# Kernel optimization log

Hardware: AMD Instinct MI355X
Metric: run time of the kernel (lower is better)

## Reference

```python
import jax, jax.numpy as jnp
import numpy as np

N = 50000      # nodes (particles)
E = 1600000    # edges
G = 2000       # graphs (jets)
NEG_SLOPE = 0.2

def setup_inputs() -> dict:
    key = jax.random.key(0)
    ks = jax.random.split(key, 18)
    p = lambda k, s: (jax.random.normal(k, s, jnp.float32) * 0.1)
    return {
        'x': jax.random.normal(ks[0], (N, 3), jnp.float32),
        'edge_index': jax.random.randint(ks[1], (2, E), 0, N, dtype=jnp.int64),
        'batch': jnp.sort(jax.random.randint(ks[2], (N,), 0, G, dtype=jnp.int64)),
        'W1': p(ks[3], (3, 128)),  'a1s': p(ks[4], (4, 32)),  'a1d': p(ks[5], (4, 32)),  'b1': p(ks[6], (128,)),
        'W2': p(ks[7], (128, 128)),'a2s': p(ks[8], (4, 32)),  'a2d': p(ks[9], (4, 32)),  'b2': p(ks[10], (128,)),
        'W3': p(ks[11], (128, 32)),'a3s': p(ks[12], (1, 32)), 'a3d': p(ks[13], (1, 32)), 'b3': p(ks[14], (32,)),
        'Wh': p(ks[15], (32, 2)),  'bh': p(ks[16], (2,)),
    }

def gat_conv(x, src, dst, W, a_src, a_dst, b, concat):
    """PyG GATConv (eval mode): gather-score-softmax-scatter over edges (src->dst)."""
    n = x.shape[0]
    H, C = a_src.shape
    h = (x @ W).reshape(n, H, C)                         # [N,H,C]
    es = jnp.sum(h * a_src, axis=-1)                     # [N,H] source scores
    ed = jnp.sum(h * a_dst, axis=-1)                     # [N,H] dest scores
    e = jax.nn.leaky_relu(es[src] + ed[dst], NEG_SLOPE)  # [E,H]
    # neighbor-wise (per destination node) stable softmax
    m = jax.ops.segment_max(e, dst, num_segments=n)      # [N,H]
    m = jax.lax.stop_gradient(jnp.where(jnp.isfinite(m), m, 0.0))
    w = jnp.exp(e - m[dst])
    z = jax.ops.segment_sum(w, dst, num_segments=n)      # [N,H]
    alpha = w / (z[dst] + 1e-16)                         # [E,H]
    out = jax.ops.segment_sum(h[src] * alpha[:, :, None], dst, num_segments=n)  # [N,H,C]
    out = out.reshape(n, H * C) if concat else out.mean(axis=1)
    return out + b

def reference(x, edge_index, batch, W1, a1s, a1d, b1, W2, a2s, a2d, b2,
              W3, a3s, a3d, b3, Wh, bh):
    n = x.shape[0]
    loops = jnp.arange(n, dtype=edge_index.dtype)        # add_self_loops=True
    src = jnp.concatenate([edge_index[0], loops])
    dst = jnp.concatenate([edge_index[1], loops])
    h = jax.nn.elu(gat_conv(x, src, dst, W1, a1s, a1d, b1, True))
    h = jax.nn.elu(gat_conv(h, src, dst, W2, a2s, a2d, b2, True))
    h = jax.nn.elu(gat_conv(h, src, dst, W3, a3s, a3d, b3, False))
    cnt = jax.ops.segment_sum(jnp.ones((n,), h.dtype), batch, num_segments=G)
    pooled = jax.ops.segment_sum(h, batch, num_segments=G) / jnp.maximum(cnt, 1.0)[:, None]
    return pooled @ Wh + bh                              # [G, n_classes]
```

## Files before the change

kernel.cpp:

```cpp
#include <hip/hip_runtime.h>

#define CAP 80
#define NXCD 8
#define SUBW 128
#define NSUBR 49
#define SQC 96
#define QCAPB 512
#define CHUNK 2048

typedef int vint4 __attribute__((ext_vector_type(4)));
__device__ __forceinline__ vint4 ntload_i4(const int* p){ return __builtin_nontemporal_load((const vint4*)p); }

__device__ __forceinline__ float lrelu02(float x){ return x > 0.f ? x : 0.2f*x; }
__device__ __forceinline__ float eluf(float x){ return x > 0.f ? x : (__expf(x)-1.f); }
__device__ __forceinline__ unsigned short f2bf(float x){
  unsigned u = __float_as_uint(x);
  u += 0x7fffu + ((u >> 16) & 1u);
  return (unsigned short)(u >> 16);
}
__device__ __forceinline__ float bf2f(unsigned short b){
  return __uint_as_float(((unsigned)b) << 16);
}

__global__ void radix_proj1_kernel(const int* __restrict__ src, const int* __restrict__ dst,
                                   int E, int n, int nrb, int RW, int qcap,
                                   int* __restrict__ gcur, int2* __restrict__ qbuf,
                                   const float* __restrict__ x, const float* __restrict__ W,
                                   const float* __restrict__ as_, const float* __restrict__ ad_,
                                   unsigned short* __restrict__ hout, float* __restrict__ es,
                                   float* __restrict__ ed){
  if ((int)blockIdx.x < nrb){
    __shared__ int2 q[NXCD][QCAPB];
    __shared__ int qc[NXCD];
    __shared__ int qbase[NXCD];
    int t = threadIdx.x;
    if (t < NXCD) qc[t] = 0;
    __syncthreads();
    int e0 = blockIdx.x*CHUNK + t*8;
    if (e0 + 8 <= E){
      vint4 d40 = ntload_i4(dst + e0), d41 = ntload_i4(dst + e0 + 4);
      vint4 s40 = ntload_i4(src + e0), s41 = ntload_i4(src + e0 + 4);
      int dd[8] = {d40[0],d40[1],d40[2],d40[3],d41[0],d41[1],d41[2],d41[3]};
      int ss[8] = {s40[0],s40[1],s40[2],s40[3],s41[0],s41[1],s41[2],s41[3]};
      #pragma unroll
      for (int k = 0; k < 8; ++k){
        int qi = min(dd[k] / RW, NXCD-1);
        int pos = atomicAdd(&qc[qi], 1);
        if (pos < QCAPB) q[qi][pos] = make_int2(ss[k], dd[k]);
      }
    } else {
      for (int e = e0; e < E; ++e){
        int d = dst[e];
        int qi = min(d / RW, NXCD-1);
        int pos = atomicAdd(&qc[qi], 1);
        if (pos < QCAPB) q[qi][pos] = make_int2(src[e], d);
      }
    }
    __syncthreads();
    if (t < NXCD) qbase[t] = atomicAdd(&gcur[t], min(qc[t], QCAPB));
    __syncthreads();
    #pragma unroll
    for (int qi = 0; qi < NXCD; ++qi){
      int cq = min(qc[qi], QCAPB);
      int2* gq = qbuf + (size_t)qi*qcap;
      int b0 = qbase[qi];
      for (int i = t; i < cq; i += 256)
        if (b0 + i < qcap) gq[b0 + i] = q[qi][i];
    }
  } else {
    __shared__ float xs[2][3];
    int node0 = ((int)blockIdx.x - nrb) * 2;
    int t = threadIdx.x;
    if (t < 6){
      int nn = node0 + t/3;
      xs[t/3][t%3] = (nn < n) ? x[(size_t)nn*3 + t%3] : 0.f;
    }
    __syncthreads();
    int node = node0 + t / 128;
    int o = t % 128;
    if (node >= n) return;
    const float* xr = xs[t / 128];
    float acc = 0.f;
    #pragma unroll
    for (int k = 0; k < 3; ++k) acc = fmaf(xr[k], W[k*128 + o], acc);
    hout[(size_t)node*128 + o] = f2bf(acc);
    float ts = acc * as_[o];
    float td = acc * ad_[o];
    #pragma unroll
    for (int m = 16; m >= 1; m >>= 1){
      ts += __shfl_xor(ts, m);
      td += __shfl_xor(td, m);
    }
    if ((o & 31) == 0){
      es[node*4 + (o>>5)] = ts;
      ed[node*4 + (o>>5)] = td;
    }
  }
}

__global__ void radix_sub_kernel(const int2* __restrict__ qbuf, const int* __restrict__ gcur,
                                 int qcap, int bpr, int scap,
                                 int* __restrict__ scnt, int2* __restrict__ sbuf){
  __shared__ int2 q[NSUBR][SQC];
  __shared__ int qc[NSUBR];
  __shared__ int qb[NSUBR];
  int r  = blockIdx.x / bpr;
  int bi = blockIdx.x % bpr;
  int t = threadIdx.x;
  if (t < NSUBR) qc[t] = 0;
  __syncthreads();
  int len = min(gcur[r], qcap);
  int i0 = bi*CHUNK + t*8;
  const int2* qg = qbuf + (size_t)r*qcap;
  #pragma unroll
  for (int k = 0; k < 8; ++k){
    int i = i0 + k;
    if (i < len){
      int2 e = qg[i];
      int qi = (e.y >> 7) - r*NSUBR;
      int pos = atomicAdd(&qc[qi], 1);
      if (pos < SQC) q[qi][pos] = e;
    }
  }
  __syncthreads();
  if (t < NSUBR){
    int c = min(qc[t], SQC);
    qb[t] = c ? atomicAdd(&scnt[r*NSUBR + t], c) : 0;
  }
  __syncthreads();
  for (int qi = 0; qi < NSUBR; ++qi){
    int cq = min(qc[qi], SQC);
    if (!cq) continue;
    int2* gq = sbuf + (size_t)(r*NSUBR + qi)*scap;
    int b0 = qb[qi];
    for (int i = t; i < cq; i += 256)
      if (b0 + i < scap) gq[b0 + i] = q[qi][i];
  }
}

__global__ void bucket_csr_kernel(const int2* __restrict__ sbuf, const int* __restrict__ scnt,
                                  int scap, unsigned short* __restrict__ col,
                                  int* __restrict__ deg, int n){
  __shared__ unsigned short colS[SUBW*CAP];
  __shared__ int cur[SUBW];
  int sb = blockIdx.x;
  int t = threadIdx.x;
  if (t < SUBW) cur[t] = 0;
  __syncthreads();
  int len = min(scnt[sb], scap);
  const int2* sq = sbuf + (size_t)sb*scap;
  for (int i = t; i < len; i += 256){
    int2 e = sq[i];
    int r = e.y & (SUBW-1);
    int slot = atomicAdd(&cur[r], 1);
    if (slot < CAP) colS[r*CAP + slot] = (unsigned short)e.x;
  }
  __syncthreads();
  int base = sb*SUBW;
  int nb = min(SUBW, n - base);
  const uint4* srcp = (const uint4*)colS;
  uint4* dstp = (uint4*)(col + (size_t)base*CAP);
  for (int i = t; i < nb*10; i += 256) dstp[i] = srcp[i];
  if (t < nb) deg[base + t] = min(cur[t], CAP);
}

template<int OUT, int NPT, int H>
__global__ void proj_tiled_kernel(const float* __restrict__ x, const float* __restrict__ W,
                                  const float* __restrict__ as_, const float* __restrict__ ad_,
                                  unsigned short* __restrict__ hout, float* __restrict__ es,
                                  float* __restrict__ ed, int n){
  constexpr int OG = OUT / 4;
  constexpr int NG = 256 / OG;
  constexpr int NODES = NG * NPT;
  __shared__ float xs[128][NODES + 1];
  int node0 = blockIdx.x * NODES;
  int t = threadIdx.x;
  for (int i = t; i < NODES*32; i += 256){
    int nl = i >> 5, kc = i & 31;
    int nn = node0 + nl;
    float4 v = make_float4(0.f,0.f,0.f,0.f);
    if (nn < n) v = *(const float4*)(x + (size_t)nn*128 + kc*4);
    xs[kc*4+0][nl] = v.x;
    xs[kc*4+1][nl] = v.y;
    xs[kc*4+2][nl] = v.z;
    xs[kc*4+3][nl] = v.w;
  }
  __syncthreads();
  int og = t % OG;
  int ng = t / OG;
  float acc[NPT][4];
  #pragma unroll
  for (int p = 0; p < NPT; ++p){ acc[p][0]=0.f; acc[p][1]=0.f; acc[p][2]=0.f; acc[p][3]=0.f; }
  const float* wp = W + og*4;
  #pragma unroll 4
  for (int k = 0; k < 128; ++k){
    float4 w = *(const float4*)(wp + (size_t)k*OUT);
    #pragma unroll
    for (int p = 0; p < NPT; ++p){
      float xv = xs[k][ng*NPT + p];
      acc[p][0] = fmaf(xv, w.x, acc[p][0]);
      acc[p][1] = fmaf(xv, w.y, acc[p][1]);
      acc[p][2] = fmaf(xv, w.z, acc[p][2]);
      acc[p][3] = fmaf(xv, w.w, acc[p][3]);
    }
  }
  int o = og*4;
  float as0 = as_[o], as1 = as_[o+1], as2 = as_[o+2], as3 = as_[o+3];
  float ad0 = ad_[o], ad1 = ad_[o+1], ad2 = ad_[o+2], ad3 = ad_[o+3];
  #pragma unroll
  for (int p = 0; p < NPT; ++p){
    int node = node0 + ng*NPT + p;
    float ts = acc[p][0]*as0 + acc[p][1]*as1 + acc[p][2]*as2 + acc[p][3]*as3;
    float td = acc[p][0]*ad0 + acc[p][1]*ad1 + acc[p][2]*ad2 + acc[p][3]*ad3;
    #pragma unroll
    for (int m = 4; m >= 1; m >>= 1){
      ts += __shfl_xor(ts, m);
      td += __shfl_xor(td, m);
    }
    if (node < n){
      ushort4 hb;
      hb.x = f2bf(acc[p][0]); hb.y = f2bf(acc[p][1]);
      hb.z = f2bf(acc[p][2]); hb.w = f2bf(acc[p][3]);
      *(ushort4*)(hout + (size_t)node*OUT + o) = hb;
      if ((og & 7) == 0){
        int head = og >> 3;
        es[node*H + head] = ts;
        ed[node*H + head] = td;
      }
    }
  }
}

__global__ void agg128_kernel(const unsigned short* __restrict__ h, const float* __restrict__ es,
                              const float* __restrict__ ed, const int* __restrict__ deg,
                              const unsigned short* __restrict__ col, const float* __restrict__ bias,
                              float* __restrict__ out, int n){
  int node = blockIdx.x*4 + (threadIdx.x >> 6);
  int lane = threadIdx.x & 63;
  if (node >= n) return;
  int beg = node*CAP;
  int end = beg + min(deg[node], CAP);
  int head = lane >> 4;
  float ed_h = ed[node*4 + head];
  float a0 = 0.f, a1 = 0.f, z = 0.f;
  int e = beg;
  for (; e + 16 <= end; e += 16){
    int sm = (int)col[e + (lane & 15)];
    float wm = __expf(lrelu02(es[sm*4 + head] + ed_h));
    int sk[16]; float wk[16]; unsigned u[16];
    #pragma unroll
    for (int k = 0; k < 16; ++k) sk[k] = __shfl(sm, k);
    #pragma unroll
    for (int k = 0; k < 16; ++k) wk[k] = __shfl(wm, (lane & 48) + k);
    #pragma unroll
    for (int k = 0; k < 16; ++k) u[k] = *(const unsigned*)(h + (size_t)sk[k]*128 + 2*lane);
    #pragma unroll
    for (int k = 0; k < 16; ++k){
      z += wk[k];
      a0 = fmaf(wk[k], __uint_as_float(u[k] << 16), a0);
      a1 = fmaf(wk[k], __uint_as_float(u[k] & 0xffff0000u), a1);
    }
  }
  for (; e < end; ++e){
    int s = col[e];
    float w = __expf(lrelu02(es[s*4 + head] + ed_h));
    unsigned u = *(const unsigned*)(h + (size_t)s*128 + 2*lane);
    z += w;
    a0 = fmaf(w, __uint_as_float(u << 16), a0);
    a1 = fmaf(w, __uint_as_float(u & 0xffff0000u), a1);
  }
  {
    float w = __expf(lrelu02(es[node*4 + head] + ed_h));
    unsigned u = *(const unsigned*)(h + (size_t)node*128 + 2*lane);
    z += w;
    a0 = fmaf(w, __uint_as_float(u << 16), a0);
    a1 = fmaf(w, __uint_as_float(u & 0xffff0000u), a1);
  }
  float inv = 1.f / (z + 1e-16f);
  int o = 2*lane;
  float2 r;
  r.x = eluf(a0*inv + bias[o]);
  r.y = eluf(a1*inv + bias[o+1]);
  *(float2*)(out + (size_t)node*128 + o) = r;
}

__global__ void agg32_kernel(const unsigned short* __restrict__ h, const float* __restrict__ es,
                             const float* __restrict__ ed, const int* __restrict__ deg,
                             const unsigned short* __restrict__ col, const float* __restrict__ bias,
                             float* __restrict__ out, int n){
  int node = blockIdx.x*4 + (threadIdx.x >> 6);
  int lane = threadIdx.x & 63;
  if (node >= n) return;
  int beg = node*CAP;
  int end = beg + min(deg[node], CAP);
  int half = lane >> 5;
  int c = lane & 31;
  float ed0 = ed[node];
  float a0 = 0.f, z = 0.f;
  int e = beg;
  for (; e + 16 <= end; e += 16){
    uint4 c0 = *(const uint4*)(col + e + 8*half);
    unsigned cw[4] = {c0.x,c0.y,c0.z,c0.w};
    int s[8]; float q[8], hv[8];
    #pragma unroll
    for (int k = 0; k < 4; ++k){ s[2*k] = cw[k] & 0xffffu; s[2*k+1] = cw[k] >> 16; }
    #pragma unroll
    for (int k = 0; k < 8; ++k) q[k] = es[s[k]];
    #pragma unroll
    for (int k = 0; k < 8; ++k) hv[k] = bf2f(h[(size_t)s[k]*32 + c]);
    #pragma unroll
    for (int k = 0; k < 8; ++k){
      float w = __expf(lrelu02(q[k] + ed0));
      z += w;
      a0 = fmaf(w, hv[k], a0);
    }
  }
  for (; e + 2 <= end; e += 2){
    int s = col[e + half];
    float w = __expf(lrelu02(es[s] + ed0));
    float hv = bf2f(h[(size_t)s*32 + c]);
    z += w;
    a0 = fmaf(w, hv, a0);
  }
  if (e < end && half == 0){
    int s = col[e];
    float w = __expf(lrelu02(es[s] + ed0));
    float hv = bf2f(h[(size_t)s*32 + c]);
    z += w;
    a0 = fmaf(w, hv, a0);
  }
  a0 += __shfl_xor(a0, 32);
  z  += __shfl_xor(z, 32);
  {
    float w = __expf(lrelu02(es[node] + ed0));
    float hv = bf2f(h[(size_t)node*32 + c]);
    z += w;
    a0 = fmaf(w, hv, a0);
  }
  if (half == 0){
    float inv = 1.f / (z + 1e-16f);
    out[(size_t)node*32 + c] = eluf(a0*inv + bias[c]);
  }
}

__global__ void pool_kernel(const float* __restrict__ h3, const int* __restrict__ batch,
                            float* __restrict__ pooled, float* __restrict__ cnt, int n){
  int i = blockIdx.x*blockDim.x + threadIdx.x;
  int node = i >> 5, c = i & 31;
  if (node >= n) return;
  int g = batch[node];
  atomicAdd(&pooled[g*32 + c], h3[(size_t)node*32 + c]);
  if (c == 0) atomicAdd(&cnt[g], 1.f);
}

__global__ void head_kernel(const float* __restrict__ pooled, const float* __restrict__ cnt,
                            const float* __restrict__ Wh, const float* __restrict__ bh,
                            float* __restrict__ out, int G){
  int g = blockIdx.x*blockDim.x + threadIdx.x;
  if (g >= G) return;
  float inv = 1.f / fmaxf(cnt[g], 1.f);
  float o0 = bh[0], o1 = bh[1];
  #pragma unroll
  for (int c = 0; c < 32; ++c){
    float p = pooled[g*32 + c] * inv;
    o0 = fmaf(p, Wh[c*2+0], o0);
    o1 = fmaf(p, Wh[c*2+1], o1);
  }
  out[g*2+0] = o0;
  out[g*2+1] = o1;
}

extern "C" void kernel_launch(void* const* d_in, const int* in_sizes, int n_in,
                              void* d_out, int out_size, void* d_ws, size_t ws_size,
                              hipStream_t stream){
  const float* x   = (const float*)d_in[0];
  const int*   ei  = (const int*)d_in[1];
  const int* batch = (const int*)d_in[2];
  const float* W1  = (const float*)d_in[3];
  const float* a1s = (const float*)d_in[4];
  const float* a1d = (const float*)d_in[5];
  const float* b1  = (const float*)d_in[6];
  const float* W2  = (const float*)d_in[7];
  const float* a2s = (const float*)d_in[8];
  const float* a2d = (const float*)d_in[9];
  const float* b2  = (const float*)d_in[10];
  const float* W3  = (const float*)d_in[11];
  const float* a3s = (const float*)d_in[12];
  const float* a3d = (const float*)d_in[13];
  const float* b3  = (const float*)d_in[14];
  const float* Wh  = (const float*)d_in[15];
  const float* bh  = (const float*)d_in[16];
  const int n = in_sizes[0] / 3;
  const int E = in_sizes[1] / 2;
  const int G = out_size / 2;
  float* out = (float*)d_out;

  const int RW   = NSUBR * SUBW;
  const int NSB  = (n + SUBW - 1) / SUBW;
  const int qcap = E/NXCD * 5/4 + 4096;
  const int scap = (int)((long long)E*SUBW/n * 5/4) + 512;

  char* p = (char*)d_ws;
  auto alloc = [&](size_t bytes)->char*{ char* r = p; p += (bytes + 255) & ~(size_t)255; return r; };
  float* buf_x            = (float*)alloc((size_t)n*128*4);
  unsigned short* buf_h   = (unsigned short*)alloc((size_t)n*128*2);
  float* es     = (float*)alloc((size_t)n*4*4);
  float* ed     = (float*)alloc((size_t)n*4*4);
  float* pooled = (float*)alloc((size_t)G*33*4);
  float* cnt    = pooled + (size_t)G*32;
  int* deg      = (int*)alloc((size_t)n*4);
  unsigned short* col = (unsigned short*)alloc((size_t)n*CAP*2);
  int* gcur     = (int*)alloc(NXCD*4);
  int* scnt     = (int*)alloc((size_t)(NXCD*NSUBR)*4);
  int2* qbuf    = (int2*)alloc((size_t)NXCD*qcap*8);
  int2* sbuf    = (int2*)alloc((size_t)NXCD*NSUBR*scap*8);

  const int* srcr = ei;
  const int* dstr = ei + E;

  hipMemsetAsync(gcur, 0, NXCD*4, stream);
  hipMemsetAsync(scnt, 0, (size_t)(NXCD*NSUBR)*4, stream);
  hipMemsetAsync(pooled, 0, (size_t)G*33*4, stream);

  int nrb = (E + CHUNK - 1) / CHUNK;
  int proj_blocks = (n + 1) / 2;
  radix_proj1_kernel<<<nrb + proj_blocks, 256, 0, stream>>>(
      srcr, dstr, E, n, nrb, RW, qcap, gcur, qbuf, x, W1, a1s, a1d, buf_h, es, ed);
  int bpr = (qcap + CHUNK - 1) / CHUNK;
  radix_sub_kernel<<<NXCD*bpr, 256, 0, stream>>>(qbuf, gcur, qcap, bpr, scap, scnt, sbuf);
  bucket_csr_kernel<<<NSB, 256, 0, stream>>>(sbuf, scnt, scap, col, deg, n);

  agg128_kernel<<<(n+3)/4, 256, 0, stream>>>(buf_h, es, ed, deg, col, b1, buf_x, n);
  proj_tiled_kernel<128,4,4><<<(n+31)/32, 256, 0, stream>>>(buf_x, W2, a2s, a2d, buf_h, es, ed, n);
  agg128_kernel<<<(n+3)/4, 256, 0, stream>>>(buf_h, es, ed, deg, col, b2, buf_x, n);
  proj_tiled_kernel<32,2,1><<<(n+63)/64, 256, 0, stream>>>(buf_x, W3, a3s, a3d, buf_h, es, ed, n);
  agg32_kernel<<<(n+3)/4, 256, 0, stream>>>(buf_h, es, ed, deg, col, b3, buf_x, n);

  pool_kernel<<<((n*32)+255)/256, 256, 0, stream>>>(buf_x, batch, pooled, cnt, n);
  head_kernel<<<(G+255)/256, 256, 0, stream>>>(pooled, cnt, Wh, bh, out, G);
}
```

Baseline: 352.5 us.

## Precompute attention weights in LDS and vectorize column loads in agg128

The 128-wide aggregation kernel now computes each edge's exp-score once per (edge, head) in a first pass, storing the weights in shared memory and reducing the normalizer with cross-lane shuffles. A second pass reads the column indices as vector loads and the weights from shared memory, replacing the previous per-edge shuffles and the scalar tail loop by padding to multiples of 16. The CSR build now zero-fills the column scratch so padded slots read node 0 with weight zero. The gain is fewer redundant exp computations and shuffles, at the cost of a shared-memory pass, an extra barrier-free phase, and gathers for padded edges.

After: 318.7 us. 9.6% less time.

```diff
diff --git a/kernel.cpp b/kernel.cpp
--- a/kernel.cpp
+++ b/kernel.cpp
@@ -145,6 +145,11 @@
   __shared__ int cur[SUBW];
   int sb = blockIdx.x;
   int t = threadIdx.x;
+  {
+    uint4 zz = make_uint4(0,0,0,0);
+    uint4* cz = (uint4*)colS;
+    for (int i = t; i < SUBW*CAP*2/16; i += 256) cz[i] = zz;
+  }
   if (t < SUBW) cur[t] = 0;
   __syncthreads();
   int len = min(scnt[sb], scap);
@@ -235,39 +240,55 @@
                               const float* __restrict__ ed, const int* __restrict__ deg,
                               const unsigned short* __restrict__ col, const float* __restrict__ bias,
                               float* __restrict__ out, int n){
-  int node = blockIdx.x*4 + (threadIdx.x >> 6);
+  __shared__ float wsS[4][4][CAP];
+  int wv = threadIdx.x >> 6;
+  int node = blockIdx.x*4 + wv;
   int lane = threadIdx.x & 63;
   if (node >= n) return;
   int beg = node*CAP;
-  int end = beg + min(deg[node], CAP);
+  int degN = min(deg[node], CAP);
+  int degR = (degN + 15) & ~15;
+  int eh = lane >> 2, hh = lane & 3;
+  float edh = ed[node*4 + hh];
+  float zp = 0.f;
+  for (int base = 0; base < degR; base += 16){
+    int e = base + eh;
+    float w = 0.f;
+    if (e < degN){
+      int s = (int)col[beg + e];
+      w = __expf(lrelu02(es[s*4 + hh] + edh));
+    }
+    wsS[wv][hh][e] = w;
+    zp += w;
+  }
+  #pragma unroll
+  for (int m = 4; m <= 32; m <<= 1) zp += __shfl_xor(zp, m);
   int head = lane >> 4;
-  float ed_h = ed[node*4 + head];
-  float a0 = 0.f, a1 = 0.f, z = 0.f;
-  int e = beg;
-  for (; e + 16 <= end; e += 16){
-    int sm = (int)col[e + (lane & 15)];
-    float wm = __expf(lrelu02(es[sm*4 + head] + ed_h));
-    int sk[16]; float wk[16]; unsigned u[16];
-    #pragma unroll
-    for (int k = 0; k < 16; ++k) sk[k] = __shfl(sm, k);
-    #pragma unroll
-    for (int k = 0; k < 16; ++k) wk[k] = __shfl(wm, (lane & 48) + k);
-    #pragma unroll
-    for (int k = 0; k < 16; ++k) u[k] = *(const unsigned*)(h + (size_t)sk[k]*128 + 2*lane);
+  float z = __shfl(zp, head);
+  float ed_h = __shfl(edh, head);
+  float a0 = 0.f, a1 = 0.f;
+  const unsigned short* colp = col + beg;
+  for (int base = 0; base < degR; base += 16){
+    uint4 c0 = *(const uint4*)(colp + base);
+    uint4 c1 = *(const uint4*)(colp + base + 8);
+    unsigned cw[8] = {c0.x,c0.y,c0.z,c0.w,c1.x,c1.y,c1.z,c1.w};
+    int s[16];
+    #pragma unroll
+    for (int k = 0; k < 8; ++k){ s[2*k] = cw[k] & 0xffffu; s[2*k+1] = cw[k] >> 16; }
+    float4 w0 = *(const float4*)&wsS[wv][head][base];
+    float4 w1 = *(const float4*)&wsS[wv][head][base+4];
+    float4 w2 = *(const float4*)&wsS[wv][head][base+8];
+    float4 w3 = *(const float4*)&wsS[wv][head][base+12];
+    float wk[16] = {w0.x,w0.y,w0.z,w0.w, w1.x,w1.y,w1.z,w1.w,
+                    w2.x,w2.y,w2.z,w2.w, w3.x,w3.y,w3.z,w3.w};
+    unsigned u[16];
+    #pragma unroll
+    for (int k = 0; k < 16; ++k) u[k] = *(const unsigned*)(h + (size_t)s[k]*128 + 2*lane);
     #pragma unroll
     for (int k = 0; k < 16; ++k){
-      z += wk[k];
       a0 = fmaf(wk[k], __uint_as_float(u[k] << 16), a0);
       a1 = fmaf(wk[k], __uint_as_float(u[k] & 0xffff0000u), a1);
     }
-  }
-  for (; e < end; ++e){
-    int s = col[e];
-    float w = __expf(lrelu02(es[s*4 + head] + ed_h));
-    unsigned u = *(const unsigned*)(h + (size_t)s*128 + 2*lane);
-    z += w;
-    a0 = fmaf(w, __uint_as_float(u << 16), a0);
-    a1 = fmaf(w, __uint_as_float(u & 0xffff0000u), a1);
   }
   {
     float w = __expf(lrelu02(es[node*4 + head] + ed_h));
```
